# Optimization experiments

Hardware: AMD Instinct MI355X
Metric: run time of the kernel (lower is better)

Reference implementation:

```python
import jax, jax.numpy as jnp
import numpy as np

EPS = 1e-5

# Binary (1-bit) quantization with straight-through estimator (hardtanh STE),
# matching brevitas BINARY quant for both weights and activations.
@jax.custom_vjp
def binarize(x):
    return jnp.where(x >= 0, 1.0, -1.0).astype(x.dtype)

def _bin_fwd(x):
    return binarize(x), x

def _bin_bwd(x, g):
    return (g * (jnp.abs(x) <= 1.0).astype(g.dtype),)

binarize.defvjp(_bin_fwd, _bin_bwd)


def setup_inputs() -> dict:
    key = jax.random.key(0)
    ks = jax.random.split(key, 12)
    B = 65536
    x = jax.random.uniform(ks[0], (B, 1, 28, 28), jnp.float32)          # MNIST-like input in [0,1]
    W0 = jax.random.uniform(ks[1], (1024, 784), jnp.float32, -1.0, 1.0)  # uniform_(-1,1) init
    Wh = jax.random.uniform(ks[2], (2, 1024, 1024), jnp.float32, -1.0, 1.0)
    WL = jax.random.uniform(ks[3], (10, 1024), jnp.float32, -1.0, 1.0)
    bn_gamma = jax.random.uniform(ks[4], (3, 1024), jnp.float32, 0.5, 1.5)
    bn_beta = 0.1 * jax.random.normal(ks[5], (3, 1024), jnp.float32)
    bn_mean = 0.1 * jax.random.normal(ks[6], (3, 1024), jnp.float32)
    bn_var = jax.random.uniform(ks[7], (3, 1024), jnp.float32, 0.5, 1.5)
    bnL_gamma = jax.random.uniform(ks[8], (10,), jnp.float32, 0.5, 1.5)
    bnL_beta = 0.1 * jax.random.normal(ks[9], (10,), jnp.float32)
    bnL_mean = 0.1 * jax.random.normal(ks[10], (10,), jnp.float32)
    bnL_var = jax.random.uniform(ks[11], (10,), jnp.float32, 0.5, 1.5)
    return {"x": x, "W0": W0, "Wh": Wh, "WL": WL,
            "bn_gamma": bn_gamma, "bn_beta": bn_beta, "bn_mean": bn_mean, "bn_var": bn_var,
            "bnL_gamma": bnL_gamma, "bnL_beta": bnL_beta, "bnL_mean": bnL_mean, "bnL_var": bnL_var}


def reference(x, W0, Wh, WL, bn_gamma, bn_beta, bn_mean, bn_var,
              bnL_gamma, bnL_beta, bnL_mean, bnL_var):
    B = x.shape[0]
    h = x.reshape(B, -1)            # flatten: [B, 784]
    h = 2.0 * h - 1.0               # map [0,1] -> [-1,1]
    h = binarize(h)                 # input quant (1-bit BINARY)
    Ws = [W0, Wh[0], Wh[1]]
    for i in range(3):
        h = h @ binarize(Ws[i]).T   # binary-weight GEMM: [B,1024]
        inv_std = bn_gamma[i] / jnp.sqrt(bn_var[i] + EPS)
        h = (h - bn_mean[i]) * inv_std + bn_beta[i]   # BatchNorm1d (inference)
        h = binarize(h)             # binary activation quant
        # Dropout is identity in eval mode
    h = h @ binarize(WL).T          # last quant linear: [B,10]
    inv_std = bnL_gamma / jnp.sqrt(bnL_var + EPS)
    h = (h - bnL_mean) * inv_std + bnL_beta
    return h
```

## Files before the change

### kernel.cpp

```cpp
#include <hip/hip_runtime.h>
#include <hip/hip_bf16.h>
#include <stdint.h>

#define EPSF 1e-5f

typedef __attribute__((ext_vector_type(4))) int i32x4;
typedef __attribute__((ext_vector_type(8))) int i32x8;
typedef __attribute__((ext_vector_type(16))) float f32x16;
typedef __attribute__((ext_vector_type(16))) char c8x16;

__device__ __forceinline__ void gld_lds16(const void* g, void* l) {
  __builtin_amdgcn_global_load_lds((const __attribute__((address_space(1))) void*)g,
                                   (__attribute__((address_space(3))) void*)l, 16, 0, 0);
}

__device__ __forceinline__ i32x8 dup8(i32x4 t) {
  i32x8 a;
  a[0] = t[0]; a[1] = t[1]; a[2] = t[2]; a[3] = t[3];
  a[4] = t[0]; a[5] = t[1]; a[6] = t[2]; a[7] = t[3];
  return a;
}

#define MFMA_FP4(a, b, c) \
  __builtin_amdgcn_mfma_scale_f32_32x32x64_f8f6f4((a), (b), (c), 4, 4, 0, 0x7F7F7F7F, 0, 0x7F7F7F7F)

__global__ void k_probe(unsigned char* __restrict__ T, float* __restrict__ lam_inv) {
  const int l = threadIdx.x;
  const int half = l >> 5, c31 = l & 31;
  const int byteidx = c31 >> 1;
  const int dw = byteidx >> 2;
  const int sh = (byteidx & 3) * 8 + (c31 & 1) * 4;
  const int hot = 0x2 << sh;
#pragma unroll
  for (int pa = 0; pa < 2; ++pa) {
#pragma unroll
    for (int pb = 0; pb < 2; ++pb) {
      i32x8 a = (i32x8)0, b = (i32x8)0;
      if (half == pa) { a[dw] = hot; a[dw + 4] = hot; }
      if (half == pb) { b[dw] = hot; b[dw + 4] = hot; }
      f32x16 c = (f32x16)0.0f;
      c = MFMA_FP4(a, b, c);
#pragma unroll
      for (int r = 0; r < 16; ++r) {
        if (c[r] != 0.0f) {
          const int row = (r & 3) + 8 * (r >> 2) + 4 * half;
          T[pb * 32 + c31] = (unsigned char)(pa * 16 + (row >> 1) + 32 * (row & 1));
        }
      }
    }
  }
  i32x8 a1;
#pragma unroll
  for (int j = 0; j < 8; ++j) a1[j] = 0x22222222;
  f32x16 c = (f32x16)0.0f;
  c = MFMA_FP4(a1, a1, c);
  if (l == 0) *lam_inv = __fdiv_rn(64.0f, c[0]);
}

__global__ void k_pack(const float* __restrict__ src, unsigned char* __restrict__ dst,
                       int Ksrc, float thr) {
  int t = blockIdx.x * 256 + threadIdx.x;
  int row = t >> 5, ch = t & 31;
  int g = ch >> 1, jb = (ch & 1) << 4;
  int c0 = g * 64 + jb, c1 = c0 + 32;
  c8x16 o = (c8x16)0;
  const float* p = src + (size_t)row * Ksrc;
  const bool v0 = (c0 + 16) <= Ksrc;
  const bool v1 = (c1 + 16) <= Ksrc;
  float lo[16], hi[16];
  if (v0) {
    *(float4*)(lo + 0) = *(const float4*)(p + c0 + 0);
    *(float4*)(lo + 4) = *(const float4*)(p + c0 + 4);
    *(float4*)(lo + 8) = *(const float4*)(p + c0 + 8);
    *(float4*)(lo + 12) = *(const float4*)(p + c0 + 12);
  }
  if (v1) {
    *(float4*)(hi + 0) = *(const float4*)(p + c1 + 0);
    *(float4*)(hi + 4) = *(const float4*)(p + c1 + 4);
    *(float4*)(hi + 8) = *(const float4*)(p + c1 + 8);
    *(float4*)(hi + 12) = *(const float4*)(p + c1 + 12);
  }
#pragma unroll
  for (int e = 0; e < 16; ++e) {
    unsigned nl = v0 ? ((lo[e] >= thr) ? 2u : 10u) : 0u;
    unsigned nh = v1 ? ((hi[e] >= thr) ? 2u : 10u) : 0u;
    o[e] = (char)(nl | (nh << 4));
  }
  *(c8x16*)(dst + (size_t)t * 16) = o;
}

__global__ void k_packW(const float* __restrict__ W0, const float* __restrict__ Wh,
                        const unsigned char* __restrict__ T, unsigned char* __restrict__ dstbase) {
  const int y = blockIdx.y;
  const float* src = (y == 0) ? W0 : (Wh + (size_t)(y - 1) * 1048576);
  const int Ksrc = (y == 0) ? 784 : 1024;
  unsigned char* dst = dstbase + (size_t)y * 524288;
  int t = blockIdx.x * 256 + threadIdx.x;
  int w = t >> 5, g = (t >> 1) & 15, h = t & 1;
  const float* p = src + (size_t)w * Ksrc + g * 64;
  const int base = g * 64;
  c8x16 o;
#pragma unroll
  for (int b = 0; b < 16; ++b) {
    unsigned byte = 0;
#pragma unroll
    for (int n = 0; n < 2; ++n) {
      int k = T[h * 32 + 2 * b + n];
      int col = base + k;
      unsigned nib = 0;
      if (col < Ksrc) nib = (p[k] >= 0.0f) ? 2u : 10u;
      byte |= nib << (4 * n);
    }
    o[b] = (char)byte;
  }
  *(c8x16*)(dst + (size_t)w * 512 + g * 32 + h * 16) = o;
}

__global__ void k_prep(const float* __restrict__ bn_gamma, const float* __restrict__ bn_var,
                       const float* __restrict__ bnL_gamma, const float* __restrict__ bnL_var,
                       const float* __restrict__ WL,
                       float* __restrict__ invstd3, float* __restrict__ invstdL,
                       char* __restrict__ WLb) {
  int j = threadIdx.x;
#pragma unroll
  for (int i = 0; i < 3; ++i) {
    int idx = i * 1024 + j;
    invstd3[idx] = __fdiv_rn(bn_gamma[idx], __fsqrt_rn(__fadd_rn(bn_var[idx], EPSF)));
  }
  if (j < 10) invstdL[j] = __fdiv_rn(bnL_gamma[j], __fsqrt_rn(__fadd_rn(bnL_var[j], EPSF)));
#pragma unroll
  for (int r = 0; r < 16; ++r) {
    char v = 0;
    if (r < 10) v = (WL[r * 1024 + j] >= 0.0f) ? (char)1 : (char)-1;
    WLb[r * 1024 + j] = v;
  }
}

template <int OUT_I8>
__global__ __launch_bounds__(256, 2)
void gemm_bin(const unsigned char* __restrict__ A, const unsigned char* __restrict__ Bt,
              unsigned char* __restrict__ Cb,
              const float* __restrict__ mean, const float* __restrict__ beta,
              const float* __restrict__ invstd, const float* __restrict__ lam_inv) {
  __shared__ char lds[32768];
  const int tid = threadIdx.x;
  const int lane = tid & 63;
  const int wave = tid >> 6;
  const int d = blockIdx.x;
  const int xcd = d & 7;
  const int idx = d >> 3;
  const int bm = xcd * 64 + (idx >> 3);
  const int bn = idx & 7;
  const int wm = wave >> 1, wn = wave & 1;
  const int h = lane >> 5, r31 = lane & 31;

  const int srow = tid >> 3;
  const int schunk = ((tid & 7) ^ (srow & 7)) << 4;
  const unsigned char* gA = A + (size_t)(bm * 128 + srow) * 512 + schunk;
  const unsigned char* gB = Bt + (size_t)(bn * 128 + srow) * 512 + schunk;
  const int lwoff = (tid & ~63) * 16;

  const float li = *lam_inv;

  f32x16 acc00 = (f32x16)0.0f, acc01 = (f32x16)0.0f;
  f32x16 acc10 = (f32x16)0.0f, acc11 = (f32x16)0.0f;

  const int arow = (wm * 64 + r31) * 128;
  const int brow = 16384 + (wn * 64 + r31) * 128;

#pragma unroll
  for (int t = 0; t < 4; ++t) {
    const int ko = t * 128;
#pragma unroll
    for (int i = 0; i < 4; ++i) {
      gld_lds16(gA + ko + i * 16384, lds + lwoff + i * 4096);
      gld_lds16(gB + ko + i * 16384, lds + 16384 + lwoff + i * 4096);
    }
    __syncthreads();
#pragma unroll
    for (int s = 0; s < 4; ++s) {
      const int slot = (((s << 1) + h) ^ (r31 & 7)) << 4;
      i32x8 a0 = dup8(*(const i32x4*)(lds + arow + slot));
      i32x8 a1 = dup8(*(const i32x4*)(lds + arow + 4096 + slot));
      i32x8 b0 = dup8(*(const i32x4*)(lds + brow + slot));
      i32x8 b1 = dup8(*(const i32x4*)(lds + brow + 4096 + slot));
      acc00 = MFMA_FP4(a0, b0, acc00);
      acc01 = MFMA_FP4(a0, b1, acc01);
      acc10 = MFMA_FP4(a1, b0, acc10);
      acc11 = MFMA_FP4(a1, b1, acc11);
    }
    __syncthreads();
  }

  const int rbase = bm * 128 + wm * 64 + 4 * h;
  const int c0 = bn * 128 + wn * 64 + r31;
  const float mu0 = mean[c0], is0 = invstd[c0], be0 = beta[c0];
  const float mu1 = mean[c0 + 32], is1 = invstd[c0 + 32], be1 = beta[c0 + 32];
  const int cb = bn * 64 + wn * 32 + r31;
#pragma unroll
  for (int mt = 0; mt < 2; ++mt) {
    const f32x16 a0 = (mt == 0) ? acc00 : acc10;
    const f32x16 a1 = (mt == 0) ? acc01 : acc11;
#pragma unroll
    for (int r = 0; r < 16; ++r) {
      const int row = rbase + mt * 32 + (r & 3) + 8 * (r >> 2);
      float y0 = __fadd_rn(__fmul_rn(__fsub_rn(__fmul_rn(a0[r], li), mu0), is0), be0);
      float y1 = __fadd_rn(__fmul_rn(__fsub_rn(__fmul_rn(a1[r], li), mu1), is1), be1);
      if (OUT_I8) {
        Cb[(size_t)row * 1024 + c0] = (y0 >= 0.0f) ? 1 : 0xFF;
        Cb[(size_t)row * 1024 + c0 + 32] = (y1 >= 0.0f) ? 1 : 0xFF;
      } else {
        unsigned nl = (y0 >= 0.0f) ? 2u : 10u;
        unsigned nh = (y1 >= 0.0f) ? 2u : 10u;
        Cb[(size_t)row * 512 + cb] = (unsigned char)(nl | (nh << 4));
      }
    }
  }
}

__global__ __launch_bounds__(256, 2)
void gemm_fin(const char* __restrict__ A, const char* __restrict__ BtL,
              float* __restrict__ out,
              const float* __restrict__ meanL, const float* __restrict__ betaL,
              const float* __restrict__ invstdL) {
  constexpr int K = 1024;
  __shared__ char sA[128 * 64];
  __shared__ char sB[16 * 64];
  const int tid = threadIdx.x;
  const int lane = tid & 63;
  const int wave = tid >> 6;
  const int bm = blockIdx.x;

  const int sr = tid >> 2;
  const int csrc = ((tid & 3) ^ (sr & 3)) << 4;
  const char* gA = A + (size_t)(bm * 128 + sr) * K + csrc;
  const char* gB = BtL + (size_t)sr * K + csrc;
  char* lA = sA + (tid & ~63) * 16;
  char* lB = sB;

  const int slot = ((lane >> 4) ^ (lane & 3)) << 4;
  const char* rA = sA + (wave * 32 + (lane & 15)) * 64 + slot;
  const char* rB = sB + (lane & 15) * 64 + slot;

  i32x4 acc0 = (i32x4)0, acc1 = (i32x4)0;

  for (int k0 = 0; k0 < K; k0 += 64) {
    gld_lds16(gA, lA);
    gld_lds16(gA + (size_t)64 * K, lA + 4096);
    if (tid < 64) gld_lds16(gB, lB);
    gA += 64;
    gB += 64;
    __syncthreads();
    i32x4 af0 = *(const i32x4*)(rA);
    i32x4 af1 = *(const i32x4*)(rA + 16 * 64);
    i32x4 b0 = *(const i32x4*)(rB);
    acc0 = __builtin_amdgcn_mfma_i32_16x16x64_i8(af0, b0, acc0, 0, 0, 0);
    acc1 = __builtin_amdgcn_mfma_i32_16x16x64_i8(af1, b0, acc1, 0, 0, 0);
    __syncthreads();
  }

  const int col = lane & 15;
  if (col < 10) {
    const float mu = meanL[col], is = invstdL[col], be = betaL[col];
    const int r0 = bm * 128 + wave * 32 + ((lane >> 4) << 2);
#pragma unroll
    for (int m = 0; m < 2; ++m) {
      const i32x4 a = (m == 0) ? acc0 : acc1;
#pragma unroll
      for (int j = 0; j < 4; ++j) {
        const int row = r0 + m * 16 + j;
        out[(size_t)row * 10 + col] = __fadd_rn(__fmul_rn(__fsub_rn((float)a[j], mu), is), be);
      }
    }
  }
}

extern "C" void kernel_launch(void* const* d_in, const int* in_sizes, int n_in,
                              void* d_out, int out_size, void* d_ws, size_t ws_size,
                              hipStream_t stream) {
  const float* x = (const float*)d_in[0];
  const float* W0 = (const float*)d_in[1];
  const float* Wh = (const float*)d_in[2];
  const float* WL = (const float*)d_in[3];
  const float* bn_gamma = (const float*)d_in[4];
  const float* bn_beta = (const float*)d_in[5];
  const float* bn_mean = (const float*)d_in[6];
  const float* bn_var = (const float*)d_in[7];
  const float* bnL_gamma = (const float*)d_in[8];
  const float* bnL_beta = (const float*)d_in[9];
  const float* bnL_mean = (const float*)d_in[10];
  const float* bnL_var = (const float*)d_in[11];
  float* out = (float*)d_out;

  char* ws = (char*)d_ws;
  unsigned char* X0f4 = (unsigned char*)ws;
  unsigned char* X1f4 = (unsigned char*)(ws + 33554432);
  unsigned char* Xi8 = (unsigned char*)(ws + 67108864);
  char* wbase = ws + 134217728;
  unsigned char* Wf4 = (unsigned char*)wbase;
  char* WLb = wbase + 3 * 524288;
  float* invstd3 = (float*)(wbase + 3 * 524288 + 16384);
  float* invstdL = invstd3 + 3 * 1024;
  float* lam_inv = invstdL + 16;
  unsigned char* T = (unsigned char*)(lam_inv + 16);

  hipLaunchKernelGGL(k_prep, dim3(1), dim3(1024), 0, stream,
                     bn_gamma, bn_var, bnL_gamma, bnL_var, WL, invstd3, invstdL, WLb);
  hipLaunchKernelGGL(k_probe, dim3(1), dim3(64), 0, stream, T, lam_inv);
  hipLaunchKernelGGL(k_packW, dim3(128, 3), dim3(256), 0, stream, W0, Wh, T, Wf4);
  hipLaunchKernelGGL(k_pack, dim3(8192), dim3(256), 0, stream, x, X0f4, 784, 0.5f);

  hipLaunchKernelGGL((gemm_bin<0>), dim3(4096), dim3(256), 0, stream, X0f4, Wf4, X1f4,
                     bn_mean, bn_beta, invstd3, lam_inv);
  hipLaunchKernelGGL((gemm_bin<0>), dim3(4096), dim3(256), 0, stream, X1f4, Wf4 + 524288, X0f4,
                     bn_mean + 1024, bn_beta + 1024, invstd3 + 1024, lam_inv);
  hipLaunchKernelGGL((gemm_bin<1>), dim3(4096), dim3(256), 0, stream, X0f4, Wf4 + 2 * 524288, Xi8,
                     bn_mean + 2048, bn_beta + 2048, invstd3 + 2048, lam_inv);
  hipLaunchKernelGGL(gemm_fin, dim3(512), dim3(256), 0, stream, (const char*)Xi8, (const char*)WLb,
                     out, bnL_mean, bnL_beta, invstdL);
}
```

Measured before the change: 197.9 us.

## Use two waves per GEMM block with 128x64 per-wave tiles

Cuts the binary GEMM block from four waves to two. Each wave now computes a 128x64 output tile (4x2 MFMA accumulators) instead of 64x64, and the global-to-LDS copy loop is doubled so 128 threads still fill the same 32KB tile. This increases A-fragment reuse per wave and lowers LDS read traffic per MFMA. The cost is more accumulator registers, fewer waves to hide latency, and twice as many load instructions per thread.

```diff
diff --git a/kernel.cpp b/kernel.cpp
--- a/kernel.cpp
+++ b/kernel.cpp
@@ -137,7 +137,7 @@
 }
 
 template <int OUT_I8>
-__global__ __launch_bounds__(256, 2)
+__global__ __launch_bounds__(128, 2)
 void gemm_bin(const unsigned char* __restrict__ A, const unsigned char* __restrict__ Bt,
               unsigned char* __restrict__ Cb,
               const float* __restrict__ mean, const float* __restrict__ beta,
@@ -151,7 +151,6 @@
   const int idx = d >> 3;
   const int bm = xcd * 64 + (idx >> 3);
   const int bn = idx & 7;
-  const int wm = wave >> 1, wn = wave & 1;
   const int h = lane >> 5, r31 = lane & 31;
 
   const int srow = tid >> 3;
@@ -162,50 +161,54 @@
 
   const float li = *lam_inv;
 
-  f32x16 acc00 = (f32x16)0.0f, acc01 = (f32x16)0.0f;
-  f32x16 acc10 = (f32x16)0.0f, acc11 = (f32x16)0.0f;
-
-  const int arow = (wm * 64 + r31) * 128;
-  const int brow = 16384 + (wn * 64 + r31) * 128;
+  f32x16 acc[4][2];
+#pragma unroll
+  for (int m = 0; m < 4; ++m)
+#pragma unroll
+    for (int n = 0; n < 2; ++n) acc[m][n] = (f32x16)0.0f;
+
+  const int browb = 16384 + (wave * 64 + r31) * 128;
 
 #pragma unroll
   for (int t = 0; t < 4; ++t) {
     const int ko = t * 128;
 #pragma unroll
-    for (int i = 0; i < 4; ++i) {
-      gld_lds16(gA + ko + i * 16384, lds + lwoff + i * 4096);
-      gld_lds16(gB + ko + i * 16384, lds + 16384 + lwoff + i * 4096);
+    for (int i = 0; i < 8; ++i) {
+      gld_lds16(gA + ko + i * 8192, lds + lwoff + i * 2048);
+      gld_lds16(gB + ko + i * 8192, lds + 16384 + lwoff + i * 2048);
     }
     __syncthreads();
 #pragma unroll
     for (int s = 0; s < 4; ++s) {
       const int slot = (((s << 1) + h) ^ (r31 & 7)) << 4;
-      i32x8 a0 = dup8(*(const i32x4*)(lds + arow + slot));
-      i32x8 a1 = dup8(*(const i32x4*)(lds + arow + 4096 + slot));
-      i32x8 b0 = dup8(*(const i32x4*)(lds + brow + slot));
-      i32x8 b1 = dup8(*(const i32x4*)(lds + brow + 4096 + slot));
-      acc00 = MFMA_FP4(a0, b0, acc00);
-      acc01 = MFMA_FP4(a0, b1, acc01);
-      acc10 = MFMA_FP4(a1, b0, acc10);
-      acc11 = MFMA_FP4(a1, b1, acc11);
+      i32x8 af[4], bf[2];
+#pragma unroll
+      for (int m = 0; m < 4; ++m)
+        af[m] = dup8(*(const i32x4*)(lds + (m * 32 + r31) * 128 + slot));
+#pragma unroll
+      for (int n = 0; n < 2; ++n)
+        bf[n] = dup8(*(const i32x4*)(lds + browb + n * 4096 + slot));
+#pragma unroll
+      for (int m = 0; m < 4; ++m)
+#pragma unroll
+        for (int n = 0; n < 2; ++n)
+          acc[m][n] = MFMA_FP4(af[m], bf[n], acc[m][n]);
     }
     __syncthreads();
   }
 
-  const int rbase = bm * 128 + wm * 64 + 4 * h;
-  const int c0 = bn * 128 + wn * 64 + r31;
+  const int c0 = bn * 128 + wave * 64 + r31;
   const float mu0 = mean[c0], is0 = invstd[c0], be0 = beta[c0];
   const float mu1 = mean[c0 + 32], is1 = invstd[c0 + 32], be1 = beta[c0 + 32];
-  const int cb = bn * 64 + wn * 32 + r31;
-#pragma unroll
-  for (int mt = 0; mt < 2; ++mt) {
-    const f32x16 a0 = (mt == 0) ? acc00 : acc10;
-    const f32x16 a1 = (mt == 0) ? acc01 : acc11;
+  const int cb = bn * 64 + wave * 32 + r31;
+#pragma unroll
+  for (int m = 0; m < 4; ++m) {
+    const int rbase = bm * 128 + m * 32 + 4 * h;
 #pragma unroll
     for (int r = 0; r < 16; ++r) {
-      const int row = rbase + mt * 32 + (r & 3) + 8 * (r >> 2);
-      float y0 = __fadd_rn(__fmul_rn(__fsub_rn(__fmul_rn(a0[r], li), mu0), is0), be0);
-      float y1 = __fadd_rn(__fmul_rn(__fsub_rn(__fmul_rn(a1[r], li), mu1), is1), be1);
+      const int row = rbase + (r & 3) + 8 * (r >> 2);
+      float y0 = __fadd_rn(__fmul_rn(__fsub_rn(__fmul_rn(acc[m][0][r], li), mu0), is0), be0);
+      float y1 = __fadd_rn(__fmul_rn(__fsub_rn(__fmul_rn(acc[m][1][r], li), mu1), is1), be1);
       if (OUT_I8) {
         Cb[(size_t)row * 1024 + c0] = (y0 >= 0.0f) ? 1 : 0xFF;
         Cb[(size_t)row * 1024 + c0 + 32] = (y1 >= 0.0f) ? 1 : 0xFF;
@@ -310,11 +313,11 @@
   hipLaunchKernelGGL(k_packW, dim3(128, 3), dim3(256), 0, stream, W0, Wh, T, Wf4);
   hipLaunchKernelGGL(k_pack, dim3(8192), dim3(256), 0, stream, x, X0f4, 784, 0.5f);
 
-  hipLaunchKernelGGL((gemm_bin<0>), dim3(4096), dim3(256), 0, stream, X0f4, Wf4, X1f4,
+  hipLaunchKernelGGL((gemm_bin<0>), dim3(4096), dim3(128), 0, stream, X0f4, Wf4, X1f4,
                      bn_mean, bn_beta, invstd3, lam_inv);
-  hipLaunchKernelGGL((gemm_bin<0>), dim3(4096), dim3(256), 0, stream, X1f4, Wf4 + 524288, X0f4,
+  hipLaunchKernelGGL((gemm_bin<0>), dim3(4096), dim3(128), 0, stream, X1f4, Wf4 + 524288, X0f4,
                      bn_mean + 1024, bn_beta + 1024, invstd3 + 1024, lam_inv);
-  hipLaunchKernelGGL((gemm_bin<1>), dim3(4096), dim3(256), 0, stream, X0f4, Wf4 + 2 * 524288, Xi8,
+  hipLaunchKernelGGL((gemm_bin<1>), dim3(4096), dim3(128), 0, stream, X0f4, Wf4 + 2 * 524288, Xi8,
                      bn_mean + 2048, bn_beta + 2048, invstd3 + 2048, lam_inv);
   hipLaunchKernelGGL(gemm_fin, dim3(512), dim3(256), 0, stream, (const char*)Xi8, (const char*)WLb,
                      out, bnL_mean, bnL_beta, invstdL);
```

Result: slower. 219.4 us (+10.8%).
